# Kernel optimization log

Measured on AMD Instinct MI355X. Metric: run time of the kernel, lower is better.

Reference implementation:

```python
import jax, jax.numpy as jnp
import numpy as np

B, D, E, G, P, H = 8192, 2048, 8, 4, 512, 192
T, DT, TAU, VTH, VRESET = 20, 0.001, 0.02, 0.5, 0.0
DELTA0, KTOP, KROUTE, PREDW = 7.0, 32, 2, 0.1


def setup_inputs() -> dict:
    key = jax.random.key(0)
    ks = jax.random.split(key, 12)
    s = 0.02
    return {
        "query_embedding": jax.random.normal(ks[0], (B, D), jnp.float32),
        "Wg": jax.random.normal(ks[1], (2, E), jnp.float32) * s,
        "bg": jnp.zeros((E,), jnp.float32),
        "Wp": jax.random.normal(ks[2], (2, E), jnp.float32) * s,
        "bp": jnp.zeros((E,), jnp.float32),
        "Wgg": jax.random.normal(ks[3], (2, G), jnp.float32) * s,
        "bgg": jnp.zeros((G,), jnp.float32),
        "W1": jax.random.normal(ks[4], (E, D, P), jnp.float32) * (1.0 / np.sqrt(D)),
        "b1": jnp.zeros((E, P), jnp.float32),
        "W2": jax.random.normal(ks[5], (E, P, D), jnp.float32) * (1.0 / np.sqrt(P)),
        "b2": jnp.zeros((E, D), jnp.float32),
    }


def reference(query_embedding, Wg, bg, Wp, bp, Wgg, bgg, W1, b1, W2, b2):
    x = query_embedding  # [B, D], already embed_dim -> no pad/slice
    dtype = x.dtype

    # --- Phasor bank temporal features on per-row mean ---
    qm = jnp.mean(x, axis=-1)  # [B]
    freqs = DELTA0 * jnp.arange(1, H + 1, dtype=dtype)  # [H]
    ang = qm[:, None] * freqs[None, :]  # [B, H]
    temporal = jnp.concatenate([jnp.cos(ang), jnp.sin(ang)], axis=-1)  # [B, 2H]

    # --- Spiking attention over top-K |x| indices (LIF over T steps) ---
    topk_idx = jax.lax.top_k(jnp.abs(x), KTOP)[1]  # [B, K]
    rows = jnp.arange(B)[:, None]
    I = jnp.zeros((B, D), dtype).at[rows, topk_idx].add(1.0)  # input current [B, vocab=D]

    def lif_step(v, _):
        v = v * (1.0 - DT / TAU) + I
        spike = (v >= VTH).astype(dtype)
        v = jnp.where(spike > 0, VRESET, v)
        return v, spike

    _, spikes = jax.lax.scan(lif_step, jnp.zeros((B, D), dtype), None, length=T)
    attention_gains = jnp.mean(spikes, axis=0)  # [B, D] spike rates

    # --- Bio gating inputs ---
    gate_in = jnp.stack([jnp.mean(temporal, axis=-1), jnp.mean(attention_gains, axis=-1)], axis=-1)  # [B, 2]

    gate_logits = gate_in @ Wg + bg  # [B, E]
    gate_logits = gate_logits - PREDW * (gate_in @ Wp + bp)

    # group routing bias: experts grouped round-robin i % G
    group_logits = gate_in @ Wgg + bgg  # [B, G]
    gmap = jax.nn.one_hot(jnp.arange(E) % G, G, dtype=dtype)  # [E, G]
    gate_logits = gate_logits + group_logits @ gmap.T

    gate_weights = jax.nn.softmax(gate_logits, axis=-1)  # temperature = 1

    # top-k routing + renormalization
    _, tidx = jax.lax.top_k(gate_weights, KROUTE)
    mask = jnp.zeros_like(gate_weights).at[rows, tidx].set(1.0)
    gated = gate_weights * mask
    gate_weights = gated / (jnp.sum(gated, axis=-1, keepdims=True) + 1e-9)

    # --- Dense MLP experts (bottleneck P = hidden // 4) ---
    h = jax.nn.relu(jnp.einsum('bd,edp->ebp', x, W1) + b1[:, None, :])  # [E, B, P]
    expert_out = jnp.einsum('ebp,eph->ebh', h, W2) + b2[:, None, :]  # [E, B, D]

    # gate-weighted combine
    context = jnp.einsum('be,ebh->bh', gate_weights, expert_out)  # [B, D]
    return context
```

## Files before the change

kernel.cpp:

```cpp
#include <hip/hip_runtime.h>
#include <stdint.h>

#define NB 8192
#define ND 2048
#define NE 8
#define NG 4
#define NP 512
#define NH 192

typedef _Float16 half_t;
typedef half_t f16x8 __attribute__((ext_vector_type(8)));
typedef float f32x4 __attribute__((ext_vector_type(4)));

__device__ __forceinline__ void gload16(const void* g, void* l) {
  __builtin_amdgcn_global_load_lds(
      (const __attribute__((address_space(1))) void*)g,
      (__attribute__((address_space(3))) void*)l, 16, 0, 0);
}

__global__ __launch_bounds__(256) void k_convert(
    const float* __restrict__ x, half_t* __restrict__ xh, double* __restrict__ qm)
{
  const int b = blockIdx.x;
  const int t = threadIdx.x;
  const float* xr = x + (size_t)b * ND;
  const float4 v0 = ((const float4*)xr)[t * 2];
  const float4 v1 = ((const float4*)xr)[t * 2 + 1];
  float f[8] = {v0.x, v0.y, v0.z, v0.w, v1.x, v1.y, v1.z, v1.w};
  double s = 0.0;
  __align__(16) half_t hb[8];
#pragma unroll
  for (int i = 0; i < 8; i++) { s += (double)f[i]; hb[i] = (half_t)f[i]; }
  *reinterpret_cast<int4*>(xh + (size_t)b * ND + t * 8) = *reinterpret_cast<const int4*>(hb);

#pragma unroll
  for (int m = 32; m >= 1; m >>= 1) s += __shfl_xor(s, m);
  __shared__ double part[4];
  if ((t & 63) == 0) part[t >> 6] = s;
  __syncthreads();
  if (t == 0) qm[b] = (part[0] + part[1] + part[2] + part[3]) / (double)ND;
}

__global__ __launch_bounds__(256) void k_gate(
    const double* __restrict__ qm,
    const float* __restrict__ Wg, const float* __restrict__ bg,
    const float* __restrict__ Wp, const float* __restrict__ bp,
    const float* __restrict__ Wgg, const float* __restrict__ bgg,
    int* __restrict__ e0a, int* __restrict__ e1a,
    float* __restrict__ w0a, float* __restrict__ w1a)
{
  const int wave = threadIdx.x >> 6;
  const int lane = threadIdx.x & 63;
  const int b = blockIdx.x * 4 + wave;
  const double q = qm[b];

  double part = 0.0;
#pragma unroll
  for (int i = 0; i < 3; i++) {
    int h = lane + i * 64;
    double ang = q * (7.0 * (double)(h + 1));
    part += cos(ang) + sin(ang);
  }
#pragma unroll
  for (int m = 32; m >= 1; m >>= 1) part += __shfl_xor(part, m);
  const double tm = part / (2.0 * (double)NH);
  const double gi1 = 32.0 / 2048.0;

  double lg = -1.0e300;
  if (lane < 8) {
    const int e = lane, g = e & 3;
    lg = tm * (double)Wg[e] + gi1 * (double)Wg[NE + e] + (double)bg[e];
    lg -= 0.1 * (tm * (double)Wp[e] + gi1 * (double)Wp[NE + e] + (double)bp[e]);
    lg += tm * (double)Wgg[g] + gi1 * (double)Wgg[NG + g] + (double)bgg[g];
  }
  double mx = lg;
#pragma unroll
  for (int m = 4; m >= 1; m >>= 1) mx = fmax(mx, __shfl_xor(mx, m));
  double pe = 0.0;
  if (lane < 8) pe = exp(lg - mx);
  double ps = pe;
#pragma unroll
  for (int m = 4; m >= 1; m >>= 1) ps += __shfl_xor(ps, m);

  double lgs[8], pes[8];
#pragma unroll
  for (int e = 0; e < 8; e++) { lgs[e] = __shfl(lg, e); pes[e] = __shfl(pe, e); }

  if (lane == 0) {
    int e0 = 0;
    for (int e = 1; e < NE; e++) if (lgs[e] > lgs[e0]) e0 = e;
    int e1 = (e0 == 0) ? 1 : 0;
    for (int e = 0; e < NE; e++) if (e != e0 && lgs[e] > lgs[e1]) e1 = e;
    const double p0 = pes[e0] / ps;
    const double p1 = pes[e1] / ps;
    const double den = p0 + p1 + 1e-9;
    e0a[b] = e0; e1a[b] = e1;
    w0a[b] = (float)(p0 / den);
    w1a[b] = (float)(p1 / den);
  }
}

__global__ __launch_bounds__(256) void k_bucket(
    const int* __restrict__ e0a, const int* __restrict__ e1a,
    const float* __restrict__ w0a, const float* __restrict__ w1a,
    int* __restrict__ rowl, float* __restrict__ wl, int* __restrict__ cnt,
    int* __restrict__ pos0a, int* __restrict__ pos1a,
    int* __restrict__ rowlp, int* __restrict__ cntp)
{
  const int t = threadIdx.x;
  const int r = blockIdx.x * 256 + t;
  __shared__ int hist[16], base[16], cursor[16];
  __shared__ int histp[64], basep[64], cursorp[64];
  if (t < 16) { hist[t] = 0; cursor[t] = 0; }
  if (t < 64) { histp[t] = 0; cursorp[t] = 0; }
  __syncthreads();

  const int e0 = e0a[r], e1 = e1a[r];
  const int p = e0 * 8 + e1;
  atomicAdd(&hist[e0], 1);
  atomicAdd(&hist[8 + e1], 1);
  atomicAdd(&histp[p], 1);
  __syncthreads();
  if (t < 16) base[t] = atomicAdd(&cnt[t], hist[t]);
  if (t < 64) basep[t] = atomicAdd(&cntp[t], histp[t]);
  __syncthreads();

  int p0 = atomicAdd(&cursor[e0], 1);
  int idx0 = base[e0] + p0;
  rowl[e0 * NB + idx0] = r;
  wl[e0 * NB + idx0] = w0a[r];
  pos0a[r] = idx0;

  int p1 = atomicAdd(&cursor[8 + e1], 1);
  int idx1 = base[8 + e1] + p1;
  rowl[(8 + e1) * NB + idx1] = r;
  wl[(8 + e1) * NB + idx1] = w1a[r];
  pos1a[r] = idx1;

  int pp = atomicAdd(&cursorp[p], 1);
  rowlp[p * NB + basep[p] + pp] = r;
}

__global__ __launch_bounds__(256) void k_cvt_w(
    const float* __restrict__ W1, const float* __restrict__ W2,
    half_t* __restrict__ w1t, half_t* __restrict__ w2t)
{
  const int which = blockIdx.y;
  const int R = which ? NP : ND;
  const int C = which ? ND : NP;
  const float* src = which ? W2 : W1;
  half_t* dst = which ? w2t : w1t;
  const int tiles_c = C >> 5;
  const int tiles_per_e = (R >> 5) * tiles_c;
  int id = blockIdx.x;
  int e = id / tiles_per_e;
  int rem = id - e * tiles_per_e;
  int tr = rem / tiles_c, tc = rem - tr * tiles_c;
  __shared__ float tile[32][33];
  const int tx = threadIdx.x & 31, ty = threadIdx.x >> 5;
  const float* s = src + (size_t)e * R * C + (size_t)(tr * 32) * C + tc * 32;
#pragma unroll
  for (int i = 0; i < 4; i++)
    tile[ty + i * 8][tx] = s[(size_t)(ty + i * 8) * C + tx];
  __syncthreads();
  half_t* d = dst + (size_t)e * R * C + (size_t)(tc * 32) * R + tr * 32;
#pragma unroll
  for (int i = 0; i < 4; i++)
    d[(size_t)(ty + i * 8) * R + tx] = (half_t)tile[tx][ty + i * 8];
}

__global__ void k_prefix(const int* __restrict__ cnt, const int* __restrict__ cntp,
                         int* __restrict__ pbase,
                         int* __restrict__ i16b, int* __restrict__ i16m, int* __restrict__ n16,
                         int* __restrict__ ipp, int* __restrict__ ipm, int* __restrict__ np)
{
  if (threadIdx.x == 0 && blockIdx.x == 0) {
    int s = 0;
    for (int i = 0; i < 16; i++) { pbase[i] = s; s += cnt[i]; }
    int t = 0;
    for (int b = 0; b < 16; b++)
      for (int m0 = 0; m0 < cnt[b]; m0 += 128) { i16b[t] = b; i16m[t] = m0; t++; }
    *n16 = t;
    t = 0;
    for (int p = 0; p < 64; p++)
      for (int m0 = 0; m0 < cntp[p]; m0 += 128) { ipp[t] = p; ipm[t] = m0; t++; }
    *np = t;
  }
}

__global__ __launch_bounds__(256) void k_gemm1(
    const half_t* __restrict__ xh, const half_t* __restrict__ w1t,
    const float* __restrict__ b1,
    const int* __restrict__ rowl, const float* __restrict__ wl,
    const int* __restrict__ cnt, const int* __restrict__ pbase,
    const int* __restrict__ i16b, const int* __restrict__ i16m,
    const int* __restrict__ n16, half_t* __restrict__ Hbuf)
{
  const int wi = blockIdx.y;
  if (wi >= *n16) return;
  const int bucket = i16b[wi];
  const int m0 = i16m[wi];
  const int count = cnt[bucket];
  const int e = bucket & 7;
  const int n0 = blockIdx.x * 128;
  const int t = threadIdx.x;

  __shared__ __align__(16) half_t As[3][128 * 32];
  __shared__ __align__(16) half_t Bs[3][128 * 32];
  __shared__ int rows_s[128];
  __shared__ float ws_s[128];

  if (t < 128) {
    int mi = m0 + t;
    int idx = bucket * NB + (mi < count ? mi : m0);
    rows_s[t] = rowl[idx];
    ws_s[t] = wl[idx];
  }
  __syncthreads();

  const int w = t >> 6, lane = t & 63;
  const int c0 = w * 128 + lane, c1 = c0 + 64;
  const int row0 = c0 >> 2, ch0 = c0 & 3;
  const int row1 = c1 >> 2, ch1 = c1 & 3;
  const int sw0 = (row0 >> 1) & 3, sw1 = (row1 >> 1) & 3;
  const half_t* gA0 = xh + (size_t)rows_s[row0] * ND + ((ch0 ^ sw0) * 8);
  const half_t* gA1 = xh + (size_t)rows_s[row1] * ND + ((ch1 ^ sw1) * 8);
  const half_t* w1te = w1t + (size_t)e * NP * ND;
  const half_t* gB0 = w1te + (size_t)(n0 + row0) * ND + ((ch0 ^ sw0) * 8);
  const half_t* gB1 = w1te + (size_t)(n0 + row1) * ND + ((ch1 ^ sw1) * 8);

  const int wr = w >> 1, wc = w & 1;
  const int lrow = lane & 15, lk = lane >> 4;
  const int lko = ((lk ^ ((lrow >> 1) & 3)) * 8);

  f32x4 acc[4][4];
#pragma unroll
  for (int i = 0; i < 4; i++)
#pragma unroll
    for (int j = 0; j < 4; j++) {
      acc[i][j][0] = 0.f; acc[i][j][1] = 0.f; acc[i][j][2] = 0.f; acc[i][j][3] = 0.f;
    }

  const int NT = ND / 32;

  auto stage = [&](int bi, int tt) {
    const int kk = tt * 32;
    half_t* la = &As[bi][w * 1024];
    half_t* lb = &Bs[bi][w * 1024];
    gload16(gA0 + kk, la);
    gload16(gA1 + kk, la + 512);
    gload16(gB0 + kk, lb);
    gload16(gB1 + kk, lb + 512);
  };
  auto compute = [&](int bi) {
    f16x8 af[4], bf[4];
#pragma unroll
    for (int i = 0; i < 4; i++) {
      af[i] = *reinterpret_cast<const f16x8*>(&As[bi][(wr * 64 + i * 16 + lrow) * 32 + lko]);
      bf[i] = *reinterpret_cast<const f16x8*>(&Bs[bi][(wc * 64 + i * 16 + lrow) * 32 + lko]);
    }
#pragma unroll
    for (int mi = 0; mi < 4; mi++)
#pragma unroll
      for (int ni = 0; ni < 4; ni++)
        acc[mi][ni] = __builtin_amdgcn_mfma_f32_16x16x32_f16(af[mi], bf[ni], acc[mi][ni], 0, 0, 0);
  };

  stage(0, 0);
  stage(1, 1);
  asm volatile("s_waitcnt vmcnt(4)" ::: "memory");
  __builtin_amdgcn_s_barrier();
#pragma unroll
  for (int tt = 0; tt < NT; ++tt) {
    if (tt + 2 < NT) stage((tt + 2) % 3, tt + 2);
    compute(tt % 3);
    if (tt + 1 < NT) {
      if (tt + 2 < NT) asm volatile("s_waitcnt vmcnt(4) lgkmcnt(0)" ::: "memory");
      else             asm volatile("s_waitcnt vmcnt(0) lgkmcnt(0)" ::: "memory");
      __builtin_amdgcn_s_barrier();
    }
  }

  const int pb = pbase[bucket];
#pragma unroll
  for (int mi = 0; mi < 4; mi++) {
#pragma unroll
    for (int i = 0; i < 4; i++) {
      int lm = wr * 64 + mi * 16 + lk * 4 + i;
      if (m0 + lm < count) {
        size_t prow = (size_t)(pb + m0 + lm) * NP;
        float wcoef = ws_s[lm];
#pragma unroll
        for (int ni = 0; ni < 4; ni++) {
          int col = n0 + wc * 64 + ni * 16 + lrow;
          float v = acc[mi][ni][i] + b1[e * NP + col];
          v = v > 0.f ? v : 0.f;
          Hbuf[prow + col] = (half_t)(v * wcoef);
        }
      }
    }
  }
}

__global__ __launch_bounds__(256) void k_gemm2p(
    const half_t* __restrict__ Hbuf, const half_t* __restrict__ w2t,
    const float* __restrict__ b2,
    const int* __restrict__ rowlp, const int* __restrict__ cntp,
    const int* __restrict__ pbase,
    const int* __restrict__ pos0a, const int* __restrict__ pos1a,
    const float* __restrict__ w0a, const float* __restrict__ w1a,
    const int* __restrict__ ipp, const int* __restrict__ ipm,
    const int* __restrict__ np, float* __restrict__ out)
{
  const int wi = blockIdx.y;
  if (wi >= *np) return;
  const int p = ipp[wi];
  const int m0 = ipm[wi];
  const int count = cntp[p];
  const int e0 = p >> 3, e1 = p & 7;
  const int n0 = blockIdx.x * 128;
  const int t = threadIdx.x;

  __shared__ __align__(16) half_t As[3][128 * 32];
  __shared__ __align__(16) half_t Bs[3][128 * 32];
  __shared__ int h0_s[128], h1_s[128], rs_s[128];
  __shared__ float w0_s[128], w1_s[128];

  if (t < 128) {
    int mi = m0 + t;
    int r = rowlp[p * NB + (mi < count ? mi : m0)];
    rs_s[t] = r;
    h0_s[t] = pbase[e0] + pos0a[r];
    h1_s[t] = pbase[8 + e1] + pos1a[r];
    w0_s[t] = w0a[r];
    w1_s[t] = w1a[r];
  }
  __syncthreads();

  const int w = t >> 6, lane = t & 63;
  const int c0 = w * 128 + lane, c1 = c0 + 64;
  const int row0 = c0 >> 2, ch0 = c0 & 3;
  const int row1 = c1 >> 2, ch1 = c1 & 3;
  const int sw0 = (row0 >> 1) & 3, sw1 = (row1 >> 1) & 3;
  const half_t* w2e0 = w2t + (size_t)e0 * ND * NP;
  const half_t* w2e1 = w2t + (size_t)e1 * ND * NP;
  const half_t* gA0s0 = Hbuf + (size_t)h0_s[row0] * NP + ((ch0 ^ sw0) * 8);
  const half_t* gA1s0 = Hbuf + (size_t)h0_s[row1] * NP + ((ch1 ^ sw1) * 8);
  const half_t* gA0s1 = Hbuf + (size_t)h1_s[row0] * NP + ((ch0 ^ sw0) * 8);
  const half_t* gA1s1 = Hbuf + (size_t)h1_s[row1] * NP + ((ch1 ^ sw1) * 8);
  const half_t* gB0e0 = w2e0 + (size_t)(n0 + row0) * NP + ((ch0 ^ sw0) * 8);
  const half_t* gB1e0 = w2e0 + (size_t)(n0 + row1) * NP + ((ch1 ^ sw1) * 8);
  const half_t* gB0e1 = w2e1 + (size_t)(n0 + row0) * NP + ((ch0 ^ sw0) * 8);
  const half_t* gB1e1 = w2e1 + (size_t)(n0 + row1) * NP + ((ch1 ^ sw1) * 8);

  const int wr = w >> 1, wc = w & 1;
  const int lrow = lane & 15, lk = lane >> 4;
  const int lko = ((lk ^ ((lrow >> 1) & 3)) * 8);

  f32x4 acc[4][4];
#pragma unroll
  for (int i = 0; i < 4; i++)
#pragma unroll
    for (int j = 0; j < 4; j++) {
      acc[i][j][0] = 0.f; acc[i][j][1] = 0.f; acc[i][j][2] = 0.f; acc[i][j][3] = 0.f;
    }

  const int NT = 32;

  auto stage = [&](int bi, int tt) {
    const int kk = (tt & 15) * 32;
    half_t* la = &As[bi][w * 1024];
    half_t* lb = &Bs[bi][w * 1024];
    if (tt & 16) {
      gload16(gA0s1 + kk, la);
      gload16(gA1s1 + kk, la + 512);
      gload16(gB0e1 + kk, lb);
      gload16(gB1e1 + kk, lb + 512);
    } else {
      gload16(gA0s0 + kk, la);
      gload16(gA1s0 + kk, la + 512);
      gload16(gB0e0 + kk, lb);
      gload16(gB1e0 + kk, lb + 512);
    }
  };
  auto compute = [&](int bi) {
    f16x8 af[4], bf[4];
#pragma unroll
    for (int i = 0; i < 4; i++) {
      af[i] = *reinterpret_cast<const f16x8*>(&As[bi][(wr * 64 + i * 16 + lrow) * 32 + lko]);
      bf[i] = *reinterpret_cast<const f16x8*>(&Bs[bi][(wc * 64 + i * 16 + lrow) * 32 + lko]);
    }
#pragma unroll
    for (int mi = 0; mi < 4; mi++)
#pragma unroll
      for (int ni = 0; ni < 4; ni++)
        acc[mi][ni] = __builtin_amdgcn_mfma_f32_16x16x32_f16(af[mi], bf[ni], acc[mi][ni], 0, 0, 0);
  };

  stage(0, 0);
  stage(1, 1);
  asm volatile("s_waitcnt vmcnt(4)" ::: "memory");
  __builtin_amdgcn_s_barrier();
#pragma unroll
  for (int tt = 0; tt < NT; ++tt) {
    if (tt + 2 < NT) stage((tt + 2) % 3, tt + 2);
    compute(tt % 3);
    if (tt + 1 < NT) {
      if (tt + 2 < NT) asm volatile("s_waitcnt vmcnt(4) lgkmcnt(0)" ::: "memory");
      else             asm volatile("s_waitcnt vmcnt(0) lgkmcnt(0)" ::: "memory");
      __builtin_amdgcn_s_barrier();
    }
  }

  float b20[4], b21[4];
#pragma unroll
  for (int ni = 0; ni < 4; ni++) {
    int col = n0 + wc * 64 + ni * 16 + lrow;
    b20[ni] = b2[e0 * ND + col];
    b21[ni] = b2[e1 * ND + col];
  }
#pragma unroll
  for (int mi = 0; mi < 4; mi++) {
#pragma unroll
    for (int i = 0; i < 4; i++) {
      int lm = wr * 64 + mi * 16 + lk * 4 + i;
      if (m0 + lm < count) {
        int r = rs_s[lm];
        float wb0 = w0_s[lm], wb1 = w1_s[lm];
        float* orow = out + (size_t)r * ND;
#pragma unroll
        for (int ni = 0; ni < 4; ni++) {
          int col = n0 + wc * 64 + ni * 16 + lrow;
          orow[col] = acc[mi][ni][i] + wb0 * b20[ni] + wb1 * b21[ni];
        }
      }
    }
  }
}

extern "C" void kernel_launch(void* const* d_in, const int* in_sizes, int n_in,
                              void* d_out, int out_size, void* d_ws, size_t ws_size,
                              hipStream_t stream)
{
  const float* x   = (const float*)d_in[0];
  const float* Wg  = (const float*)d_in[1];
  const float* bg  = (const float*)d_in[2];
  const float* Wp  = (const float*)d_in[3];
  const float* bp  = (const float*)d_in[4];
  const float* Wgg = (const float*)d_in[5];
  const float* bgg = (const float*)d_in[6];
  const float* W1  = (const float*)d_in[7];
  const float* b1  = (const float*)d_in[8];
  const float* W2  = (const float*)d_in[9];
  const float* b2  = (const float*)d_in[10];
  float* out = (float*)d_out;

  char* ws = (char*)d_ws;
  size_t off = 0;
  const size_t OFF_XH   = off; off += (size_t)NB * ND * 2;
  const size_t OFF_W1T  = off; off += (size_t)NE * NP * ND * 2;
  const size_t OFF_W2T  = off; off += (size_t)NE * ND * NP * 2;
  const size_t OFF_H    = off; off += (size_t)(2 * NB + 128) * NP * 2;
  const size_t OFF_ROWL = off; off += (size_t)16 * NB * 4;
  const size_t OFF_WL   = off; off += (size_t)16 * NB * 4;
  const size_t OFF_ROWLP= off; off += (size_t)64 * NB * 4;
  const size_t OFF_CNT  = off; off += 64;
  const size_t OFF_CNTP = off; off += 256;
  const size_t OFF_PB   = off; off += 64;
  const size_t OFF_QM   = off; off += (size_t)NB * 8;
  const size_t OFF_E0   = off; off += (size_t)NB * 4;
  const size_t OFF_E1   = off; off += (size_t)NB * 4;
  const size_t OFF_W0   = off; off += (size_t)NB * 4;
  const size_t OFF_W1A  = off; off += (size_t)NB * 4;
  const size_t OFF_POS0 = off; off += (size_t)NB * 4;
  const size_t OFF_POS1 = off; off += (size_t)NB * 4;
  const size_t OFF_I16B = off; off += 1024;
  const size_t OFF_I16M = off; off += 1024;
  const size_t OFF_N16  = off; off += 64;
  const size_t OFF_IPP  = off; off += 1024;
  const size_t OFF_IPM  = off; off += 1024;
  const size_t OFF_NP   = off; off += 64;

  half_t* xh   = (half_t*)(ws + OFF_XH);
  half_t* w1t  = (half_t*)(ws + OFF_W1T);
  half_t* w2t  = (half_t*)(ws + OFF_W2T);
  half_t* Hbuf = (half_t*)(ws + OFF_H);
  int*    rowl = (int*)(ws + OFF_ROWL);
  float*  wl   = (float*)(ws + OFF_WL);
  int*    rowlp= (int*)(ws + OFF_ROWLP);
  int*    cnt  = (int*)(ws + OFF_CNT);
  int*    cntp = (int*)(ws + OFF_CNTP);
  int*    pb   = (int*)(ws + OFF_PB);
  double* qm   = (double*)(ws + OFF_QM);
  int*    e0a  = (int*)(ws + OFF_E0);
  int*    e1a  = (int*)(ws + OFF_E1);
  float*  w0a  = (float*)(ws + OFF_W0);
  float*  w1a  = (float*)(ws + OFF_W1A);
  int*    pos0a= (int*)(ws + OFF_POS0);
  int*    pos1a= (int*)(ws + OFF_POS1);
  int*    i16b = (int*)(ws + OFF_I16B);
  int*    i16m = (int*)(ws + OFF_I16M);
  int*    n16  = (int*)(ws + OFF_N16);
  int*    ipp  = (int*)(ws + OFF_IPP);
  int*    ipm  = (int*)(ws + OFF_IPM);
  int*    np   = (int*)(ws + OFF_NP);

  hipMemsetAsync(cnt, 0, 64 + 256, stream);
  k_convert<<<NB, 256, 0, stream>>>(x, xh, qm);
  k_cvt_w<<<dim3(8192, 2, 1), 256, 0, stream>>>(W1, W2, w1t, w2t);
  k_gate<<<NB / 4, 256, 0, stream>>>(qm, Wg, bg, Wp, bp, Wgg, bgg, e0a, e1a, w0a, w1a);
  k_bucket<<<NB / 256, 256, 0, stream>>>(e0a, e1a, w0a, w1a, rowl, wl, cnt,
                                         pos0a, pos1a, rowlp, cntp);
  k_prefix<<<1, 64, 0, stream>>>(cnt, cntp, pb, i16b, i16m, n16, ipp, ipm, np);
  k_gemm1<<<dim3(4, 144, 1), 256, 0, stream>>>(xh, w1t, b1, rowl, wl, cnt, pb,
                                               i16b, i16m, n16, Hbuf);
  k_gemm2p<<<dim3(16, 128, 1), 256, 0, stream>>>(Hbuf, w2t, b2, rowlp, cntp, pb,
                                                 pos0a, pos1a, w0a, w1a, ipp, ipm, np, out);
}
```

Before: 345.4 us.

## Load expert weight fragments directly from global into registers, stage only activations in LDS

Both expert GEMM kernels stop staging the weight (B) tile in shared memory. Each wave now reads its MFMA weight fragments straight from global memory into registers. Only the gathered activation tile goes through LDS, widened to a K depth of 64 with a new XOR swizzle, which halves the number of pipeline steps. The kernels also ask for 3 blocks per CU through launch bounds. This removes LDS traffic and footprint for weights, but puts global-load latency directly in the MFMA loop, and those loads share the vmcnt counter with the prefetch waits, which may serialize the pipeline.

```diff
diff --git a/kernel.cpp b/kernel.cpp
--- a/kernel.cpp
+++ b/kernel.cpp
@@ -188,7 +188,7 @@
   }
 }
 
-__global__ __launch_bounds__(256) void k_gemm1(
+__global__ __launch_bounds__(256, 3) void k_gemm1(
     const half_t* __restrict__ xh, const half_t* __restrict__ w1t,
     const float* __restrict__ b1,
     const int* __restrict__ rowl, const float* __restrict__ wl,
@@ -205,8 +205,7 @@
   const int n0 = blockIdx.x * 128;
   const int t = threadIdx.x;
 
-  __shared__ __align__(16) half_t As[3][128 * 32];
-  __shared__ __align__(16) half_t Bs[3][128 * 32];
+  __shared__ __align__(16) half_t As[3][128 * 64];
   __shared__ int rows_s[128];
   __shared__ float ws_s[128];
 
@@ -219,19 +218,20 @@
   __syncthreads();
 
   const int w = t >> 6, lane = t & 63;
-  const int c0 = w * 128 + lane, c1 = c0 + 64;
-  const int row0 = c0 >> 2, ch0 = c0 & 3;
-  const int row1 = c1 >> 2, ch1 = c1 & 3;
-  const int sw0 = (row0 >> 1) & 3, sw1 = (row1 >> 1) & 3;
-  const half_t* gA0 = xh + (size_t)rows_s[row0] * ND + ((ch0 ^ sw0) * 8);
-  const half_t* gA1 = xh + (size_t)rows_s[row1] * ND + ((ch1 ^ sw1) * 8);
-  const half_t* w1te = w1t + (size_t)e * NP * ND;
-  const half_t* gB0 = w1te + (size_t)(n0 + row0) * ND + ((ch0 ^ sw0) * 8);
-  const half_t* gB1 = w1te + (size_t)(n0 + row1) * ND + ((ch1 ^ sw1) * 8);
+  const int srow = (w << 3) + (lane >> 3);
+  const int sch = (lane & 7) ^ (lane >> 3);
+  const half_t* sa0 = xh + (size_t)rows_s[srow] * ND + sch * 8;
+  const half_t* sa1 = xh + (size_t)rows_s[32 + srow] * ND + sch * 8;
+  const half_t* sa2 = xh + (size_t)rows_s[64 + srow] * ND + sch * 8;
+  const half_t* sa3 = xh + (size_t)rows_s[96 + srow] * ND + sch * 8;
 
   const int wr = w >> 1, wc = w & 1;
   const int lrow = lane & 15, lk = lane >> 4;
-  const int lko = ((lk ^ ((lrow >> 1) & 3)) * 8);
+  const half_t* w1te = w1t + (size_t)e * NP * ND;
+  const half_t* pB0 = w1te + (size_t)(n0 + wc * 64 + 0  + lrow) * ND + lk * 8;
+  const half_t* pB1 = w1te + (size_t)(n0 + wc * 64 + 16 + lrow) * ND + lk * 8;
+  const half_t* pB2 = w1te + (size_t)(n0 + wc * 64 + 32 + lrow) * ND + lk * 8;
+  const half_t* pB3 = w1te + (size_t)(n0 + wc * 64 + 48 + lrow) * ND + lk * 8;
 
   f32x4 acc[4][4];
 #pragma unroll
@@ -241,29 +241,37 @@
       acc[i][j][0] = 0.f; acc[i][j][1] = 0.f; acc[i][j][2] = 0.f; acc[i][j][3] = 0.f;
     }
 
-  const int NT = ND / 32;
+  const int NT = ND / 64;
 
   auto stage = [&](int bi, int tt) {
-    const int kk = tt * 32;
-    half_t* la = &As[bi][w * 1024];
-    half_t* lb = &Bs[bi][w * 1024];
-    gload16(gA0 + kk, la);
-    gload16(gA1 + kk, la + 512);
-    gload16(gB0 + kk, lb);
-    gload16(gB1 + kk, lb + 512);
+    const int kk = tt * 64;
+    half_t* ld = &As[bi][t * 8];
+    gload16(sa0 + kk, ld);
+    gload16(sa1 + kk, ld + 2048);
+    gload16(sa2 + kk, ld + 4096);
+    gload16(sa3 + kk, ld + 6144);
   };
-  auto compute = [&](int bi) {
-    f16x8 af[4], bf[4];
-#pragma unroll
-    for (int i = 0; i < 4; i++) {
-      af[i] = *reinterpret_cast<const f16x8*>(&As[bi][(wr * 64 + i * 16 + lrow) * 32 + lko]);
-      bf[i] = *reinterpret_cast<const f16x8*>(&Bs[bi][(wc * 64 + i * 16 + lrow) * 32 + lko]);
-    }
-#pragma unroll
-    for (int mi = 0; mi < 4; mi++)
-#pragma unroll
-      for (int ni = 0; ni < 4; ni++)
-        acc[mi][ni] = __builtin_amdgcn_mfma_f32_16x16x32_f16(af[mi], bf[ni], acc[mi][ni], 0, 0, 0);
+  auto compute = [&](int bi, int tt) {
+#pragma unroll
+    for (int ks = 0; ks < 2; ks++) {
+      f16x8 af[4], bf[4];
+#pragma unroll
+      for (int i = 0; i < 4; i++) {
+        const int r = wr * 64 + i * 16 + lrow;
+        const int slot = (ks * 4 + lk) ^ (lrow & 7);
+        af[i] = *reinterpret_cast<const f16x8*>(&As[bi][r * 64 + slot * 8]);
+      }
+      const int ko = tt * 64 + ks * 32;
+      bf[0] = *reinterpret_cast<const f16x8*>(pB0 + ko);
+      bf[1] = *reinterpret_cast<const f16x8*>(pB1 + ko);
+      bf[2] = *reinterpret_cast<const f16x8*>(pB2 + ko);
+      bf[3] = *reinterpret_cast<const f16x8*>(pB3 + ko);
+#pragma unroll
+      for (int mi = 0; mi < 4; mi++)
+#pragma unroll
+        for (int ni = 0; ni < 4; ni++)
+          acc[mi][ni] = __builtin_amdgcn_mfma_f32_16x16x32_f16(af[mi], bf[ni], acc[mi][ni], 0, 0, 0);
+    }
   };
 
   stage(0, 0);
@@ -273,7 +281,7 @@
 #pragma unroll
   for (int tt = 0; tt < NT; ++tt) {
     if (tt + 2 < NT) stage((tt + 2) % 3, tt + 2);
-    compute(tt % 3);
+    compute(tt % 3, tt);
     if (tt + 1 < NT) {
       if (tt + 2 < NT) asm volatile("s_waitcnt vmcnt(4) lgkmcnt(0)" ::: "memory");
       else             asm volatile("s_waitcnt vmcnt(0) lgkmcnt(0)" ::: "memory");
@@ -302,7 +310,7 @@
   }
 }
 
-__global__ __launch_bounds__(256) void k_gemm2p(
+__global__ __launch_bounds__(256, 3) void k_gemm2p(
     const half_t* __restrict__ Hbuf, const half_t* __restrict__ w2t,
     const float* __restrict__ b2,
     const int* __restrict__ rowlp, const int* __restrict__ cntp,
@@ -321,8 +329,7 @@
   const int n0 = blockIdx.x * 128;
   const int t = threadIdx.x;
 
-  __shared__ __align__(16) half_t As[3][128 * 32];
-  __shared__ __align__(16) half_t Bs[3][128 * 32];
+  __shared__ __align__(16) half_t As[3][128 * 64];
   __shared__ int h0_s[128], h1_s[128], rs_s[128];
   __shared__ float w0_s[128], w1_s[128];
 
@@ -338,24 +345,29 @@
   __syncthreads();
 
   const int w = t >> 6, lane = t & 63;
-  const int c0 = w * 128 + lane, c1 = c0 + 64;
-  const int row0 = c0 >> 2, ch0 = c0 & 3;
-  const int row1 = c1 >> 2, ch1 = c1 & 3;
-  const int sw0 = (row0 >> 1) & 3, sw1 = (row1 >> 1) & 3;
+  const int srow = (w << 3) + (lane >> 3);
+  const int sch = (lane & 7) ^ (lane >> 3);
+  const half_t* sa00 = Hbuf + (size_t)h0_s[srow] * NP + sch * 8;
+  const half_t* sa01 = Hbuf + (size_t)h0_s[32 + srow] * NP + sch * 8;
+  const half_t* sa02 = Hbuf + (size_t)h0_s[64 + srow] * NP + sch * 8;
+  const half_t* sa03 = Hbuf + (size_t)h0_s[96 + srow] * NP + sch * 8;
+  const half_t* sa10 = Hbuf + (size_t)h1_s[srow] * NP + sch * 8;
+  const half_t* sa11 = Hbuf + (size_t)h1_s[32 + srow] * NP + sch * 8;
+  const half_t* sa12 = Hbuf + (size_t)h1_s[64 + srow] * NP + sch * 8;
+  const half_t* sa13 = Hbuf + (size_t)h1_s[96 + srow] * NP + sch * 8;
+
+  const int wr = w >> 1, wc = w & 1;
+  const int lrow = lane & 15, lk = lane >> 4;
   const half_t* w2e0 = w2t + (size_t)e0 * ND * NP;
   const half_t* w2e1 = w2t + (size_t)e1 * ND * NP;
-  const half_t* gA0s0 = Hbuf + (size_t)h0_s[row0] * NP + ((ch0 ^ sw0) * 8);
-  const half_t* gA1s0 = Hbuf + (size_t)h0_s[row1] * NP + ((ch1 ^ sw1) * 8);
-  const half_t* gA0s1 = Hbuf + (size_t)h1_s[row0] * NP + ((ch0 ^ sw0) * 8);
-  const half_t* gA1s1 = Hbuf + (size_t)h1_s[row1] * NP + ((ch1 ^ sw1) * 8);
-  const half_t* gB0e0 = w2e0 + (size_t)(n0 + row0) * NP + ((ch0 ^ sw0) * 8);
-  const half_t* gB1e0 = w2e0 + (size_t)(n0 + row1) * NP + ((ch1 ^ sw1) * 8);
-  const half_t* gB0e1 = w2e1 + (size_t)(n0 + row0) * NP + ((ch0 ^ sw0) * 8);
-  const half_t* gB1e1 = w2e1 + (size_t)(n0 + row1) * NP + ((ch1 ^ sw1) * 8);
-
-  const int wr = w >> 1, wc = w & 1;
-  const int lrow = lane & 15, lk = lane >> 4;
-  const int lko = ((lk ^ ((lrow >> 1) & 3)) * 8);
+  const half_t* pB00 = w2e0 + (size_t)(n0 + wc * 64 + 0  + lrow) * NP + lk * 8;
+  const half_t* pB01 = w2e0 + (size_t)(n0 + wc * 64 + 16 + lrow) * NP + lk * 8;
+  const half_t* pB02 = w2e0 + (size_t)(n0 + wc * 64 + 32 + lrow) * NP + lk * 8;
+  const half_t* pB03 = w2e0 + (size_t)(n0 + wc * 64 + 48 + lrow) * NP + lk * 8;
+  const half_t* pB10 = w2e1 + (size_t)(n0 + wc * 64 + 0  + lrow) * NP + lk * 8;
+  const half_t* pB11 = w2e1 + (size_t)(n0 + wc * 64 + 16 + lrow) * NP + lk * 8;
+  const half_t* pB12 = w2e1 + (size_t)(n0 + wc * 64 + 32 + lrow) * NP + lk * 8;
+  const half_t* pB13 = w2e1 + (size_t)(n0 + wc * 64 + 48 + lrow) * NP + lk * 8;
 
   f32x4 acc[4][4];
 #pragma unroll
@@ -365,36 +377,51 @@
       acc[i][j][0] = 0.f; acc[i][j][1] = 0.f; acc[i][j][2] = 0.f; acc[i][j][3] = 0.f;
     }
 
-  const int NT = 32;
+  const int NT = 16;
 
   auto stage = [&](int bi, int tt) {
-    const int kk = (tt & 15) * 32;
-    half_t* la = &As[bi][w * 1024];
-    half_t* lb = &Bs[bi][w * 1024];
-    if (tt & 16) {
-      gload16(gA0s1 + kk, la);
-      gload16(gA1s1 + kk, la + 512);
-      gload16(gB0e1 + kk, lb);
-      gload16(gB1e1 + kk, lb + 512);
+    const int kk = (tt & 7) * 64;
+    half_t* ld = &As[bi][t * 8];
+    if (tt & 8) {
+      gload16(sa10 + kk, ld);
+      gload16(sa11 + kk, ld + 2048);
+      gload16(sa12 + kk, ld + 4096);
+      gload16(sa13 + kk, ld + 6144);
     } else {
-      gload16(gA0s0 + kk, la);
-      gload16(gA1s0 + kk, la + 512);
-      gload16(gB0e0 + kk, lb);
-      gload16(gB1e0 + kk, lb + 512);
+      gload16(sa00 + kk, ld);
+      gload16(sa01 + kk, ld + 2048);
+      gload16(sa02 + kk, ld + 4096);
+      gload16(sa03 + kk, ld + 6144);
     }
   };
-  auto compute = [&](int bi) {
-    f16x8 af[4], bf[4];
-#pragma unroll
-    for (int i = 0; i < 4; i++) {
-      af[i] = *reinterpret_cast<const f16x8*>(&As[bi][(wr * 64 + i * 16 + lrow) * 32 + lko]);
-      bf[i] = *reinterpret_cast<const f16x8*>(&Bs[bi][(wc * 64 + i * 16 + lrow) * 32 + lko]);
-    }
-#pragma unroll
-    for (int mi = 0; mi < 4; mi++)
-#pragma unroll
-      for (int ni = 0; ni < 4; ni++)
-        acc[mi][ni] = __builtin_amdgcn_mfma_f32_16x16x32_f16(af[mi], bf[ni], acc[mi][ni], 0, 0, 0);
+  auto compute = [&](int bi, int tt) {
+#pragma unroll
+    for (int ks = 0; ks < 2; ks++) {
+      f16x8 af[4], bf[4];
+#pragma unroll
+      for (int i = 0; i < 4; i++) {
+        const int r = wr * 64 + i * 16 + lrow;
+        const int slot = (ks * 4 + lk) ^ (lrow & 7);
+        af[i] = *reinterpret_cast<const f16x8*>(&As[bi][r * 64 + slot * 8]);
+      }
+      const int ko = (tt & 7) * 64 + ks * 32;
+      if (tt & 8) {
+        bf[0] = *reinterpret_cast<const f16x8*>(pB10 + ko);
+        bf[1] = *reinterpret_cast<const f16x8*>(pB11 + ko);
+        bf[2] = *reinterpret_cast<const f16x8*>(pB12 + ko);
+        bf[3] = *reinterpret_cast<const f16x8*>(pB13 + ko);
+      } else {
+        bf[0] = *reinterpret_cast<const f16x8*>(pB00 + ko);
+        bf[1] = *reinterpret_cast<const f16x8*>(pB01 + ko);
+        bf[2] = *reinterpret_cast<const f16x8*>(pB02 + ko);
+        bf[3] = *reinterpret_cast<const f16x8*>(pB03 + ko);
+      }
+#pragma unroll
+      for (int mi = 0; mi < 4; mi++)
+#pragma unroll
+        for (int ni = 0; ni < 4; ni++)
+          acc[mi][ni] = __builtin_amdgcn_mfma_f32_16x16x32_f16(af[mi], bf[ni], acc[mi][ni], 0, 0, 0);
+    }
   };
 
   stage(0, 0);
@@ -404,7 +431,7 @@
 #pragma unroll
   for (int tt = 0; tt < NT; ++tt) {
     if (tt + 2 < NT) stage((tt + 2) % 3, tt + 2);
-    compute(tt % 3);
+    compute(tt % 3, tt);
     if (tt + 1 < NT) {
       if (tt + 2 < NT) asm volatile("s_waitcnt vmcnt(4) lgkmcnt(0)" ::: "memory");
       else             asm volatile("s_waitcnt vmcnt(0) lgkmcnt(0)" ::: "memory");
```

Result: slower. 420.9 us (+21.9%).
